# Optimization experiments

Measured on AMD Instinct MI355X. Metric: run time of the kernel, lower is better.

## Reference

```python
import jax, jax.numpy as jnp
import numpy as np

B, T, D = 2, 2048, 2048
N, KH, H = 16, 8, 128  # query heads, kv heads, head_dim
S = 2048               # cache size
EPS = 1e-6
ROPE_THETA = 1000000.0
K_MASK = -0.7 * float(np.finfo(np.float32).max)  # jax _get_large_negative(float32)


def _rms_norm(x, w):
    rms = jnp.sqrt(jnp.mean(x.astype(jnp.float32) ** 2, axis=-1, keepdims=True) + EPS)
    return (w * x / rms).astype(x.dtype)


def _rope_embeddings(positions, head_dim):
    fraction = jnp.arange(0, head_dim, 2, dtype=jnp.float32) / head_dim
    inv_freq = 1.0 / (ROPE_THETA ** fraction)
    sinusoid = jnp.einsum('BT,k->BTk', positions.astype(jnp.float32), inv_freq,
                          precision=jax.lax.Precision.HIGHEST)
    return jnp.sin(sinusoid), jnp.cos(sinusoid)


def _apply_rope(x, sin, cos):
    h = x.shape[-1] // 2
    x1, x2 = x[..., :h], x[..., h:]
    s, c = sin[:, :, None, :], cos[:, :, None, :]
    return jnp.concatenate([x1 * c - x2 * s, x2 * c + x1 * s], axis=-1).astype(x.dtype)


def _positions_from_segment_ids(seg):
    t = seg.shape[1]
    pos = jnp.arange(t, dtype=jnp.int32)[None, :] - jnp.argmax(seg, axis=1)[:, None]
    return jnp.where(seg != 0, pos, 2 ** 30)


def _num_left_pad(seg):
    return jnp.sum(jnp.cumsum(seg != 0, axis=-1) == 0, axis=-1).astype(jnp.int32)


def _attention(x, q_w, k_w, v_w, o_w, q_norm_w, k_norm_w, k_cache, v_cache,
               segment_ids, start_ind, cur_ind):
    b, t, _ = x.shape
    s = k_cache.shape[1]
    n, kh, h = q_w.shape[1], k_w.shape[1], q_w.shape[2]

    q = _rms_norm(jnp.einsum('BTD,DNH->BTNH', x, q_w), q_norm_w)  # [B,T,N,H]
    k = _rms_norm(jnp.einsum('BSD,DKH->BSKH', x, k_w), k_norm_w)  # [B,T,K,H]
    v = jnp.einsum('BSD,DKH->BSKH', x, v_w)                       # [B,T,K,H]

    start = jnp.where(start_ind < 0, _num_left_pad(segment_ids), start_ind)
    pos = _positions_from_segment_ids(segment_ids) + cur_ind
    sin, cos = _rope_embeddings(pos, h)
    q = _apply_rope(q, sin, cos)
    k = _apply_rope(k, sin, cos)

    # KV-cache update at cur_ind
    k_cache = jax.lax.dynamic_update_slice(k_cache, k, (0, cur_ind, 0, 0))
    v_cache = jax.lax.dynamic_update_slice(v_cache, v, (0, cur_ind, 0, 0))

    # GQA: group query heads per kv head
    qg = q.reshape(b, t, kh, n // kh, h)
    logits = jnp.einsum('BTHGD,BSHD->BHGTS', qg, k_cache) * (h ** -0.5)

    q_pos = cur_ind + jnp.arange(t, dtype=jnp.int32)[None, :] - start[:, None]  # [B,T]
    ts = jnp.arange(s, dtype=jnp.int32)
    kv_seg = (ts[None, :] >= start[:, None]) & (ts[None, :] < cur_ind + t)      # [B,S] bool
    k_pos = ts[None, :] - start[:, None]                                        # [B,S]
    causal = k_pos[:, None, :] <= q_pos[:, :, None]                             # [B,T,S]
    # faithful to original: bool kv segment ids compared against int segment_ids
    seg_mask = kv_seg[:, None, :].astype(segment_ids.dtype) == segment_ids[:, :, None]
    final_mask = (causal & seg_mask)[:, None, None, :, :]                       # [B,1,1,T,S]

    logits = jnp.where(final_mask, logits, K_MASK)
    attn = jax.nn.softmax(logits.astype(jnp.float32), axis=-1).astype(logits.dtype)
    o = jnp.einsum('BHGTS,BSHD->BTHGD', attn, v_cache).reshape(b, t, n, h)
    return jnp.einsum('BTNH,NHD->BTD', o, o_w)


def setup_inputs() -> dict:
    key = jax.random.key(0)
    ks = jax.random.split(key, 5)
    scale = 0.02
    return {
        'x': jax.random.normal(ks[0], (B, T, D), jnp.float32),
        'q_w': jax.random.normal(ks[1], (D, N, H), jnp.float32) * scale,
        'k_w': jax.random.normal(ks[2], (D, KH, H), jnp.float32) * scale,
        'v_w': jax.random.normal(ks[3], (D, KH, H), jnp.float32) * scale,
        'o_w': jax.random.normal(ks[4], (N, H, D), jnp.float32) * scale,
        'q_norm_w': jnp.ones((H,), jnp.float32),
        'k_norm_w': jnp.ones((H,), jnp.float32),
        'k_cache': jnp.zeros((B, S, KH, H), jnp.float32),
        'v_cache': jnp.zeros((B, S, KH, H), jnp.float32),
        'segment_ids': jnp.ones((B, T), jnp.int32),
        'start_ind': jnp.zeros((B,), jnp.int32),
        'cur_ind': 0,
        'right_pads': 0,
    }


def reference(x, q_w, k_w, v_w, o_w, q_norm_w, k_norm_w, k_cache, v_cache,
              segment_ids, start_ind, cur_ind, right_pads):
    # right_pads only advances the cache write pointer (stateful side effect); it
    # does not affect the attention output.
    return _attention(x, q_w, k_w, v_w, o_w, q_norm_w, k_norm_w,
                      k_cache, v_cache, segment_ids, start_ind, cur_ind)
```

## Files before the change

kernel.cpp:

```cpp
#include <hip/hip_runtime.h>
#include <climits>
#include <math.h>

#define Bc   2
#define Tc   2048
#define Dc   2048
#define Nc   16
#define KHc  8
#define Hc   128
#define Sc   2048

constexpr float EPSc   = 1e-6f;
constexpr float SCALE2 = 0.1275174477984469f;

typedef short short8 __attribute__((ext_vector_type(8)));
typedef float float4v __attribute__((ext_vector_type(4)));

union U16x8 { uint4 u; short8 s8; unsigned short us[8]; };

__device__ __forceinline__ unsigned short f2bf(float f) {
    union { float f; unsigned u; } v; v.f = f;
    unsigned r = v.u + 0x7FFFu + ((v.u >> 16) & 1u);
    return (unsigned short)(r >> 16);
}
__device__ __forceinline__ float bf2f(unsigned short u) {
    union { unsigned u; float f; } v; v.u = ((unsigned)u) << 16;
    return v.f;
}

__global__ void meta_kernel(const int* __restrict__ seg,
                            const int* __restrict__ start_ind,
                            int* __restrict__ meta)
{
    int b = blockIdx.x;
    __shared__ int s_max, s_amax, s_nz;
    if (threadIdx.x == 0) { s_max = INT_MIN; s_amax = Tc; s_nz = Tc; }
    __syncthreads();
    int lmax = INT_MIN;
    for (int t = threadIdx.x; t < Tc; t += blockDim.x)
        lmax = max(lmax, seg[b * Tc + t]);
    atomicMax(&s_max, lmax);
    __syncthreads();
    int mv = s_max;
    int lamax = Tc, lnz = Tc;
    for (int t = threadIdx.x; t < Tc; t += blockDim.x) {
        int v = seg[b * Tc + t];
        if (v == mv) lamax = min(lamax, t);
        if (v != 0)  lnz   = min(lnz, t);
    }
    atomicMin(&s_amax, lamax);
    atomicMin(&s_nz, lnz);
    __syncthreads();
    if (threadIdx.x == 0) {
        meta[b] = s_amax;
        int st = start_ind[b];
        meta[Bc + b] = (st < 0) ? s_nz : st;
    }
}

__global__ void cast_bf16(const float* __restrict__ in, unsigned short* __restrict__ out)
{
    size_t base = ((size_t)blockIdx.x * 256 + threadIdx.x) * 8;
    float4 a = *(const float4*)&in[base];
    float4 b = *(const float4*)&in[base + 4];
    U16x8 o;
    o.us[0] = f2bf(a.x); o.us[1] = f2bf(a.y); o.us[2] = f2bf(a.z); o.us[3] = f2bf(a.w);
    o.us[4] = f2bf(b.x); o.us[5] = f2bf(b.y); o.us[6] = f2bf(b.z); o.us[7] = f2bf(b.w);
    *(uint4*)&out[base] = o.u;
}

__global__ void fill_kcache(const float* __restrict__ kc, unsigned short* __restrict__ Kall,
                            const int* __restrict__ cur_ptr)
{
    int cur = cur_ptr[0];
    size_t base = ((size_t)blockIdx.x * 256 + threadIdx.x) * 8;
    int s = (int)((base >> 10) & (Sc - 1));
    if (s >= cur && s < cur + Tc) return;
    float4 a = *(const float4*)&kc[base];
    float4 b = *(const float4*)&kc[base + 4];
    U16x8 o;
    o.us[0] = f2bf(a.x); o.us[1] = f2bf(a.y); o.us[2] = f2bf(a.z); o.us[3] = f2bf(a.w);
    o.us[4] = f2bf(b.x); o.us[5] = f2bf(b.y); o.us[6] = f2bf(b.z); o.us[7] = f2bf(b.w);
    *(uint4*)&Kall[base] = o.u;
}

__global__ __launch_bounds__(256) void transpose_cast(const float* __restrict__ in,
                                                      unsigned short* __restrict__ out,
                                                      int R, int C)
{
    __shared__ float tile[32][33];
    int tid = threadIdx.x;
    int c0 = blockIdx.x * 32, r0 = blockIdx.y * 32;
#pragma unroll
    for (int i = 0; i < 4; ++i) {
        int row = (tid >> 5) + i * 8, col = tid & 31;
        tile[row][col] = in[(size_t)(r0 + row) * C + c0 + col];
    }
    __syncthreads();
#pragma unroll
    for (int i = 0; i < 4; ++i) {
        int rowo = (tid >> 5) + i * 8, colo = tid & 31;
        out[(size_t)(c0 + rowo) * R + r0 + colo] = f2bf(tile[colo][rowo]);
    }
}

__global__ void vtrans2(const unsigned short* __restrict__ QKVh,
                        const float* __restrict__ vc,
                        unsigned short* __restrict__ Vt,
                        const int* __restrict__ cur_ptr)
{
    int gid = blockIdx.x * 256 + threadIdx.x;
    int h  = gid & 127;
    int s8 = ((gid >> 7) & 255) * 8;
    int kh = (gid >> 15) & 7;
    int b  = gid >> 18;
    int cur = cur_ptr[0], curT = cur + Tc;
    unsigned short tmp[8];
#pragma unroll
    for (int e = 0; e < 8; ++e) {
        int s = s8 + e;
        unsigned short v;
        if (s >= cur && s < curT)
            v = QKVh[(size_t)(b * Tc + (s - cur)) * 4096 + 3072 + kh * Hc + h];
        else
            v = f2bf(vc[((size_t)(b * Sc + s) * KHc + kh) * Hc + h]);
        tmp[e] = v;
    }
    *(uint4*)&Vt[(((size_t)b * KHc + kh) * Hc + h) * Sc + s8] = *(uint4*)tmp;
}

__global__ __launch_bounds__(256, 2) void gemm_mfma(const unsigned short* __restrict__ A,
                                                    const unsigned short* __restrict__ BT,
                                                    void* __restrict__ Cout,
                                                    int M, int N, int K, int out_fp32)
{
    __shared__ __align__(16) unsigned short As[128 * 32];
    __shared__ __align__(16) unsigned short Bs[128 * 32];
    int tid = threadIdx.x;
    int lane = tid & 63, w = tid >> 6;
    int quad = lane >> 4, l15 = lane & 15;
    int bm = blockIdx.y * 128, bn = blockIdx.x * 128;
    int wm = (w >> 1) * 64, wn = (w & 1) * 64;

    int srow = lane >> 2;
    int pl   = lane & 3;
    int sw   = (quad ^ ((l15 >> 1) & 3)) * 8;

    float4v acc[16];
#pragma unroll
    for (int i = 0; i < 16; ++i) acc[i] = (float4v)0.f;

    for (int k0 = 0; k0 < K; k0 += 32) {
        __syncthreads();
#pragma unroll
        for (int c = 0; c < 2; ++c) {
            int j = w * 2 + c;
            int row = j * 16 + srow;
            int pg = pl ^ ((row >> 1) & 3);
            __builtin_amdgcn_global_load_lds(
                (__attribute__((address_space(1))) void*)(A + (size_t)(bm + row) * K + k0 + pg * 8),
                (__attribute__((address_space(3))) void*)(As + j * 512), 16, 0, 0);
            __builtin_amdgcn_global_load_lds(
                (__attribute__((address_space(1))) void*)(BT + (size_t)(bn + row) * K + k0 + pg * 8),
                (__attribute__((address_space(3))) void*)(Bs + j * 512), 16, 0, 0);
        }
        __syncthreads();
        short8 af[4];
#pragma unroll
        for (int mi = 0; mi < 4; ++mi)
            af[mi] = *(const short8*)&As[(wm + mi * 16 + l15) * 32 + sw];
#pragma unroll
        for (int ni = 0; ni < 4; ++ni) {
            short8 bf = *(const short8*)&Bs[(wn + ni * 16 + l15) * 32 + sw];
#pragma unroll
            for (int mi = 0; mi < 4; ++mi)
                acc[mi * 4 + ni] = __builtin_amdgcn_mfma_f32_16x16x32_bf16(af[mi], bf, acc[mi * 4 + ni], 0, 0, 0);
        }
    }

#pragma unroll
    for (int mi = 0; mi < 4; ++mi)
#pragma unroll
        for (int ni = 0; ni < 4; ++ni)
#pragma unroll
            for (int reg = 0; reg < 4; ++reg) {
                int row = bm + wm + mi * 16 + quad * 4 + reg;
                int col = bn + wn + ni * 16 + l15;
                float v = acc[mi * 4 + ni][reg];
                if (out_fp32) ((float*)Cout)[(size_t)row * N + col] = v;
                else ((unsigned short*)Cout)[(size_t)row * N + col] = f2bf(v);
            }
}

__global__ __launch_bounds__(256) void norm_rope(unsigned short* __restrict__ QKVh,
                                                 unsigned short* __restrict__ Kall,
                                                 const float* __restrict__ qw,
                                                 const float* __restrict__ kw,
                                                 const int* __restrict__ seg,
                                                 const int* __restrict__ meta,
                                                 const int* __restrict__ cur_ptr)
{
    int rowid = blockIdx.x * 4 + (threadIdx.x >> 6);
    int lane = threadIdx.x & 63;
    int hh = rowid % 24;
    int bt = rowid / 24;
    int t = bt & (Tc - 1);
    int b = bt >> 11;
    int cur = cur_ptr[0];

    const unsigned short* in;
    unsigned short* out;
    const float* wt;
    if (hh < 16) {
        unsigned short* p = QKVh + (size_t)bt * 4096 + hh * Hc;
        in = p; out = p; wt = qw;
    } else {
        int kh = hh - 16;
        in = QKVh + (size_t)bt * 4096 + 2048 + kh * Hc;
        out = Kall + (((size_t)b * Sc + cur + t) * KHc + kh) * Hc;
        wt = kw;
    }
    float v1 = bf2f(in[lane]), v2 = bf2f(in[lane + 64]);
    float ssq = v1 * v1 + v2 * v2;
#pragma unroll
    for (int off = 1; off < 64; off <<= 1) ssq += __shfl_xor(ssq, off);
    float rinv = rsqrtf(ssq * (1.0f / Hc) + EPSc);

    int sg = seg[bt];
    long long pos = (sg != 0) ? (long long)(t - meta[b]) : (long long)(1 << 30);
    float posf = (float)(pos + (long long)cur);
    float inv_freq = exp2f(-(float)lane * (19.931568569324174f / 64.0f));
    float s, c;
    sincosf(posf * inv_freq, &s, &c);

    float n1 = wt[lane] * v1 * rinv;
    float n2 = wt[lane + 64] * v2 * rinv;
    out[lane]      = f2bf(n1 * c - n2 * s);
    out[lane + 64] = f2bf(n2 * c + n1 * s);
}

__global__ __launch_bounds__(256, 2) void flash_mfma(const unsigned short* __restrict__ Qb,
                                                     const unsigned short* __restrict__ Kall,
                                                     const unsigned short* __restrict__ Vt,
                                                     const int* __restrict__ seg,
                                                     const int* __restrict__ meta,
                                                     const int* __restrict__ cur_ptr,
                                                     unsigned short* __restrict__ Ob)
{
    __shared__ __align__(16) unsigned short Ks[64 * 128];
    __shared__ __align__(16) unsigned short Vs[128 * 64];
    __shared__ __align__(16) unsigned short Ps[128 * 72];

    int tid = threadIdx.x;
    int lane = tid & 63, w = tid >> 6;
    int quad = lane >> 4, l15 = lane & 15;
    int bid = blockIdx.x;
    int raw = bid & 15;
    int n  = (bid >> 4) & 15;
    int b  = bid >> 8;
    int qt = (b == 0) ? raw : (15 - raw);
    int kh = n >> 1;
    int cur = cur_ptr[0];
    int startb = meta[Bc + b];
    int curT = cur + Tc;
    int t0 = qt * 128 + w * 32;

    short8 qf[2][4];
#pragma unroll
    for (int mi = 0; mi < 2; ++mi)
#pragma unroll
        for (int ks = 0; ks < 4; ++ks) {
            int row = t0 + mi * 16 + l15;
            U16x8 u;
            u.u = *(const uint4*)&Qb[(size_t)(b * Tc + row) * 4096 + n * Hc + ks * 32 + quad * 8];
            qf[mi][ks] = u.s8;
        }

    int code = 0, ct[8];
#pragma unroll
    for (int mi = 0; mi < 2; ++mi)
#pragma unroll
        for (int reg = 0; reg < 4; ++reg) {
            int idx = mi * 4 + reg;
            int trow = t0 + mi * 16 + quad * 4 + reg;
            int sg = seg[b * Tc + trow];
            int cls = (sg == 0) ? 0 : ((sg == 1) ? 1 : 2);
            code |= cls << (2 * idx);
            ct[idx] = cur + trow;
        }
    bool allseg1 = (code == 0x5555);

    float lsum[8];
#pragma unroll
    for (int i = 0; i < 8; ++i) lsum[i] = 0.f;
    float4v o[16];
#pragma unroll
    for (int i = 0; i < 16; ++i) o[i] = (float4v)0.f;

    int s_end = min(Sc, cur + qt * 128 + 128);
    int nch = (s_end + 63) >> 6;

    const size_t kstride = (size_t)KHc * Hc;
    const unsigned short* kptr[4];
    unsigned short* kdst[4];
#pragma unroll
    for (int i = 0; i < 4; ++i) {
        int j = w * 4 + i;
        int row = j * 4 + (lane >> 4);
        int pl = lane & 15;
        int pg = pl ^ ((row >> 1) & 7);
        kptr[i] = Kall + (size_t)b * Sc * kstride + (size_t)row * kstride + kh * Hc + pg * 8;
        kdst[i] = Ks + j * 512;
    }
    const unsigned short* vptr[4];
    unsigned short* vdst[4];
#pragma unroll
    for (int i = 0; i < 4; ++i) {
        int j = w * 4 + i;
        int h = j * 8 + (lane >> 3);
        int pl = lane & 7;
        int pg = pl ^ ((h >> 1) & 7);
        vptr[i] = Vt + ((size_t)b * KHc + kh) * (size_t)Hc * Sc + (size_t)h * Sc + pg * 8;
        vdst[i] = Vs + j * 512;
    }
    int sw3 = (l15 >> 1) & 7;

    for (int c = 0; c < nch; ++c) {
        int s0 = c * 64;
#pragma unroll
        for (int i = 0; i < 4; ++i) {
            __builtin_amdgcn_global_load_lds(
                (__attribute__((address_space(1))) void*)(kptr[i] + (size_t)s0 * kstride),
                (__attribute__((address_space(3))) void*)kdst[i], 16, 0, 0);
            __builtin_amdgcn_global_load_lds(
                (__attribute__((address_space(1))) void*)(vptr[i] + s0),
                (__attribute__((address_space(3))) void*)vdst[i], 16, 0, 0);
        }
        __syncthreads();

        float4v sacc[2][4];
#pragma unroll
        for (int mi = 0; mi < 2; ++mi)
#pragma unroll
            for (int j = 0; j < 4; ++j) sacc[mi][j] = (float4v)0.f;
#pragma unroll
        for (int j = 0; j < 4; ++j) {
#pragma unroll
            for (int ks = 0; ks < 4; ++ks) {
                short8 kf = *(const short8*)&Ks[(j * 16 + l15) * 128 + ((ks * 4 + quad) ^ sw3) * 8];
                sacc[0][j] = __builtin_amdgcn_mfma_f32_16x16x32_bf16(qf[0][ks], kf, sacc[0][j], 0, 0, 0);
                sacc[1][j] = __builtin_amdgcn_mfma_f32_16x16x32_bf16(qf[1][ks], kf, sacc[1][j], 0, 0, 0);
            }
        }

        bool fullok = allseg1 && (s0 >= startb) && (s0 + 63 <= cur + t0) && (s0 + 63 < curT);

#pragma unroll
        for (int mi = 0; mi < 2; ++mi) {
#pragma unroll
            for (int reg = 0; reg < 4; ++reg) {
                int idx = mi * 4 + reg;
                int prow = w * 32 + mi * 16 + quad * 4 + reg;
                if (fullok) {
#pragma unroll
                    for (int j = 0; j < 4; ++j) {
                        float p = exp2f(sacc[mi][j][reg] * SCALE2);
                        lsum[idx] += p;
                        Ps[prow * 72 + j * 16 + l15] = f2bf(p);
                    }
                } else {
                    int ctv = ct[idx];
                    int clsv = (code >> (2 * idx)) & 3;
#pragma unroll
                    for (int j = 0; j < 4; ++j) {
                        int s = s0 + j * 16 + l15;
                        int kvseg = (s >= startb && s < curT) ? 1 : 0;
                        bool ok = (s <= ctv) && (clsv == kvseg);
                        float arg = ok ? sacc[mi][j][reg] * SCALE2 : -1e30f;
                        float p = exp2f(arg);
                        lsum[idx] += p;
                        Ps[prow * 72 + j * 16 + l15] = f2bf(p);
                    }
                }
            }
        }

#pragma unroll
        for (int kk = 0; kk < 2; ++kk) {
            short8 pf0 = *(const short8*)&Ps[(w * 32 + l15) * 72 + kk * 32 + quad * 8];
            short8 pf1 = *(const short8*)&Ps[(w * 32 + 16 + l15) * 72 + kk * 32 + quad * 8];
#pragma unroll
            for (int nt = 0; nt < 8; ++nt) {
                short8 vf = *(const short8*)&Vs[(nt * 16 + l15) * 64 + ((kk * 4 + quad) ^ sw3) * 8];
                o[nt]     = __builtin_amdgcn_mfma_f32_16x16x32_bf16(pf0, vf, o[nt], 0, 0, 0);
                o[8 + nt] = __builtin_amdgcn_mfma_f32_16x16x32_bf16(pf1, vf, o[8 + nt], 0, 0, 0);
            }
        }
        __syncthreads();
    }

#pragma unroll
    for (int idx = 0; idx < 8; ++idx) {
        float l = lsum[idx];
        l += __shfl_xor(l, 1);
        l += __shfl_xor(l, 2);
        l += __shfl_xor(l, 4);
        l += __shfl_xor(l, 8);
        lsum[idx] = (l > 0.f) ? (1.0f / l) : 0.f;
    }

#pragma unroll
    for (int mi = 0; mi < 2; ++mi)
#pragma unroll
        for (int reg = 0; reg < 4; ++reg) {
            float linv = lsum[mi * 4 + reg];
            int trow = t0 + mi * 16 + quad * 4 + reg;
            size_t base = ((size_t)(b * Tc + trow) * Nc + n) * Hc;
#pragma unroll
            for (int nt = 0; nt < 8; ++nt)
                Ob[base + nt * 16 + l15] = f2bf(o[mi * 8 + nt][reg] * linv);
        }
}

extern "C" void kernel_launch(void* const* d_in, const int* in_sizes, int n_in,
                              void* d_out, int out_size, void* d_ws, size_t ws_size,
                              hipStream_t stream)
{
    const float* x        = (const float*)d_in[0];
    const float* q_w      = (const float*)d_in[1];
    const float* k_w      = (const float*)d_in[2];
    const float* v_w      = (const float*)d_in[3];
    const float* o_w      = (const float*)d_in[4];
    const float* q_norm_w = (const float*)d_in[5];
    const float* k_norm_w = (const float*)d_in[6];
    const float* k_cache  = (const float*)d_in[7];
    const float* v_cache  = (const float*)d_in[8];
    const int*   seg      = (const int*)d_in[9];
    const int*   startind = (const int*)d_in[10];
    const int*   cur_ptr  = (const int*)d_in[11];
    (void)in_sizes; (void)n_in; (void)out_size; (void)ws_size;

    char* base = (char*)d_ws;
    int* meta = (int*)base;
    unsigned short* QKVh = (unsigned short*)(base + 1024);
    unsigned short* Kall = (unsigned short*)(base + 33555456);
    unsigned short* Vt   = (unsigned short*)(base + 41944064);
    unsigned short* xb   = (unsigned short*)(base + 50332672);
    unsigned short* qkvwT= (unsigned short*)(base + 67109888);
    unsigned short* owT  = (unsigned short*)(base + 83887104);
    unsigned short* Ob   = xb;

    meta_kernel<<<Bc, 256, 0, stream>>>(seg, startind, meta);

    cast_bf16<<<4096, 256, 0, stream>>>(x, xb);
    transpose_cast<<<dim3(64, 64), 256, 0, stream>>>(q_w, qkvwT, Dc, Nc * Hc);
    transpose_cast<<<dim3(32, 64), 256, 0, stream>>>(k_w, qkvwT + (size_t)2048 * 2048, Dc, KHc * Hc);
    transpose_cast<<<dim3(32, 64), 256, 0, stream>>>(v_w, qkvwT + (size_t)3072 * 2048, Dc, KHc * Hc);
    transpose_cast<<<dim3(64, 64), 256, 0, stream>>>(o_w, owT, Nc * Hc, Dc);

    gemm_mfma<<<dim3(32, 32), 256, 0, stream>>>(xb, qkvwT, QKVh, Bc * Tc, 4096, Dc, 0);

    norm_rope<<<Bc * Tc * 24 / 4, 256, 0, stream>>>(QKVh, Kall,
                                                    q_norm_w, k_norm_w, seg, meta, cur_ptr);

    fill_kcache<<<2048, 256, 0, stream>>>(k_cache, Kall, cur_ptr);
    vtrans2<<<2048, 256, 0, stream>>>(QKVh, v_cache, Vt, cur_ptr);

    flash_mfma<<<Bc * Nc * (Tc / 128), 256, 0, stream>>>(QKVh, Kall, Vt, seg, meta, cur_ptr, Ob);

    gemm_mfma<<<dim3(16, 32), 256, 0, stream>>>(Ob, owT, d_out, Bc * Tc, Dc, Nc * Hc, 1);
}
```

Baseline: 422.9 us.

## Merge prep/post kernels and transpose flash attention tiles with fp16 PV

```diff
diff --git a/kernel.cpp b/kernel.cpp
--- a/kernel.cpp
+++ b/kernel.cpp
@@ -1,4 +1,5 @@
 #include <hip/hip_runtime.h>
+#include <hip/hip_fp16.h>
 #include <climits>
 #include <math.h>
 
@@ -14,9 +15,13 @@
 constexpr float SCALE2 = 0.1275174477984469f;
 
 typedef short short8 __attribute__((ext_vector_type(8)));
+typedef _Float16 half8 __attribute__((ext_vector_type(8)));
+typedef __fp16 fp16x2 __attribute__((ext_vector_type(2)));
 typedef float float4v __attribute__((ext_vector_type(4)));
 
-union U16x8 { uint4 u; short8 s8; unsigned short us[8]; };
+union U16x8 { uint4 u; short8 s8; half8 h8; unsigned short us[8]; };
+union H2U  { fp16x2 h; unsigned u; };
+union S8H8 { short8 s; half8 h; };
 
 __device__ __forceinline__ unsigned short f2bf(float f) {
     union { float f; unsigned u; } v; v.f = f;
@@ -28,69 +33,12 @@
     return v.f;
 }
 
-__global__ void meta_kernel(const int* __restrict__ seg,
-                            const int* __restrict__ start_ind,
-                            int* __restrict__ meta)
-{
-    int b = blockIdx.x;
-    __shared__ int s_max, s_amax, s_nz;
-    if (threadIdx.x == 0) { s_max = INT_MIN; s_amax = Tc; s_nz = Tc; }
-    __syncthreads();
-    int lmax = INT_MIN;
-    for (int t = threadIdx.x; t < Tc; t += blockDim.x)
-        lmax = max(lmax, seg[b * Tc + t]);
-    atomicMax(&s_max, lmax);
-    __syncthreads();
-    int mv = s_max;
-    int lamax = Tc, lnz = Tc;
-    for (int t = threadIdx.x; t < Tc; t += blockDim.x) {
-        int v = seg[b * Tc + t];
-        if (v == mv) lamax = min(lamax, t);
-        if (v != 0)  lnz   = min(lnz, t);
-    }
-    atomicMin(&s_amax, lamax);
-    atomicMin(&s_nz, lnz);
-    __syncthreads();
-    if (threadIdx.x == 0) {
-        meta[b] = s_amax;
-        int st = start_ind[b];
-        meta[Bc + b] = (st < 0) ? s_nz : st;
-    }
-}
-
-__global__ void cast_bf16(const float* __restrict__ in, unsigned short* __restrict__ out)
-{
-    size_t base = ((size_t)blockIdx.x * 256 + threadIdx.x) * 8;
-    float4 a = *(const float4*)&in[base];
-    float4 b = *(const float4*)&in[base + 4];
-    U16x8 o;
-    o.us[0] = f2bf(a.x); o.us[1] = f2bf(a.y); o.us[2] = f2bf(a.z); o.us[3] = f2bf(a.w);
-    o.us[4] = f2bf(b.x); o.us[5] = f2bf(b.y); o.us[6] = f2bf(b.z); o.us[7] = f2bf(b.w);
-    *(uint4*)&out[base] = o.u;
-}
-
-__global__ void fill_kcache(const float* __restrict__ kc, unsigned short* __restrict__ Kall,
-                            const int* __restrict__ cur_ptr)
-{
-    int cur = cur_ptr[0];
-    size_t base = ((size_t)blockIdx.x * 256 + threadIdx.x) * 8;
-    int s = (int)((base >> 10) & (Sc - 1));
-    if (s >= cur && s < cur + Tc) return;
-    float4 a = *(const float4*)&kc[base];
-    float4 b = *(const float4*)&kc[base + 4];
-    U16x8 o;
-    o.us[0] = f2bf(a.x); o.us[1] = f2bf(a.y); o.us[2] = f2bf(a.z); o.us[3] = f2bf(a.w);
-    o.us[4] = f2bf(b.x); o.us[5] = f2bf(b.y); o.us[6] = f2bf(b.z); o.us[7] = f2bf(b.w);
-    *(uint4*)&Kall[base] = o.u;
-}
-
-__global__ __launch_bounds__(256) void transpose_cast(const float* __restrict__ in,
-                                                      unsigned short* __restrict__ out,
-                                                      int R, int C)
-{
-    __shared__ float tile[32][33];
-    int tid = threadIdx.x;
-    int c0 = blockIdx.x * 32, r0 = blockIdx.y * 32;
+__device__ __forceinline__ void tc_body(const float* __restrict__ in,
+                                        unsigned short* __restrict__ out,
+                                        int R, int C, int bx, int by, int tid,
+                                        float tile[32][33])
+{
+    int c0 = bx * 32, r0 = by * 32;
 #pragma unroll
     for (int i = 0; i < 4; ++i) {
         int row = (tid >> 5) + i * 8, col = tid & 31;
@@ -104,29 +52,67 @@
     }
 }
 
-__global__ void vtrans2(const unsigned short* __restrict__ QKVh,
-                        const float* __restrict__ vc,
-                        unsigned short* __restrict__ Vt,
-                        const int* __restrict__ cur_ptr)
-{
-    int gid = blockIdx.x * 256 + threadIdx.x;
-    int h  = gid & 127;
-    int s8 = ((gid >> 7) & 255) * 8;
-    int kh = (gid >> 15) & 7;
-    int b  = gid >> 18;
-    int cur = cur_ptr[0], curT = cur + Tc;
-    unsigned short tmp[8];
-#pragma unroll
-    for (int e = 0; e < 8; ++e) {
-        int s = s8 + e;
-        unsigned short v;
-        if (s >= cur && s < curT)
-            v = QKVh[(size_t)(b * Tc + (s - cur)) * 4096 + 3072 + kh * Hc + h];
-        else
-            v = f2bf(vc[((size_t)(b * Sc + s) * KHc + kh) * Hc + h]);
-        tmp[e] = v;
-    }
-    *(uint4*)&Vt[(((size_t)b * KHc + kh) * Hc + h) * Sc + s8] = *(uint4*)tmp;
+__global__ __launch_bounds__(256) void prep(const float* __restrict__ x,
+                                            const float* __restrict__ qw,
+                                            const float* __restrict__ kw,
+                                            const float* __restrict__ vw,
+                                            const float* __restrict__ ow,
+                                            const int* __restrict__ seg,
+                                            const int* __restrict__ start_ind,
+                                            int* __restrict__ meta,
+                                            unsigned short* __restrict__ xb,
+                                            unsigned short* __restrict__ qkvwT,
+                                            unsigned short* __restrict__ owT)
+{
+    __shared__ float tile[32][33];
+    __shared__ int s_max, s_amax, s_nz;
+    int id = blockIdx.x;
+    int tid = threadIdx.x;
+
+    if (id < Bc) {
+        int b = id;
+        if (tid == 0) { s_max = INT_MIN; s_amax = Tc; s_nz = Tc; }
+        __syncthreads();
+        int lmax = INT_MIN;
+        for (int t = tid; t < Tc; t += 256) lmax = max(lmax, seg[b * Tc + t]);
+        atomicMax(&s_max, lmax);
+        __syncthreads();
+        int mv = s_max;
+        int lamax = Tc, lnz = Tc;
+        for (int t = tid; t < Tc; t += 256) {
+            int v = seg[b * Tc + t];
+            if (v == mv) lamax = min(lamax, t);
+            if (v != 0)  lnz   = min(lnz, t);
+        }
+        atomicMin(&s_amax, lamax);
+        atomicMin(&s_nz, lnz);
+        __syncthreads();
+        if (tid == 0) {
+            meta[b] = s_amax;
+            int st = start_ind[b];
+            meta[Bc + b] = (st < 0) ? s_nz : st;
+        }
+        return;
+    }
+    id -= Bc;
+    if (id < 4096) {
+        size_t base = ((size_t)id * 256 + tid) * 8;
+        float4 a = *(const float4*)&x[base];
+        float4 b = *(const float4*)&x[base + 4];
+        U16x8 o;
+        o.us[0] = f2bf(a.x); o.us[1] = f2bf(a.y); o.us[2] = f2bf(a.z); o.us[3] = f2bf(a.w);
+        o.us[4] = f2bf(b.x); o.us[5] = f2bf(b.y); o.us[6] = f2bf(b.z); o.us[7] = f2bf(b.w);
+        *(uint4*)&xb[base] = o.u;
+        return;
+    }
+    id -= 4096;
+    if (id < 4096) { tc_body(qw, qkvwT, 2048, 2048, id & 63, id >> 6, tid, tile); return; }
+    id -= 4096;
+    if (id < 2048) { tc_body(kw, qkvwT + (size_t)2048 * 2048, 2048, 1024, id & 31, id >> 5, tid, tile); return; }
+    id -= 2048;
+    if (id < 2048) { tc_body(vw, qkvwT + (size_t)3072 * 2048, 2048, 1024, id & 31, id >> 5, tid, tile); return; }
+    id -= 2048;
+    tc_body(ow, owT, 2048, 2048, id & 63, id >> 6, tid, tile);
 }
 
 __global__ __launch_bounds__(256, 2) void gemm_mfma(const unsigned short* __restrict__ A,
@@ -192,51 +178,94 @@
             }
 }
 
-__global__ __launch_bounds__(256) void norm_rope(unsigned short* __restrict__ QKVh,
-                                                 unsigned short* __restrict__ Kall,
-                                                 const float* __restrict__ qw,
-                                                 const float* __restrict__ kw,
-                                                 const int* __restrict__ seg,
-                                                 const int* __restrict__ meta,
-                                                 const int* __restrict__ cur_ptr)
-{
-    int rowid = blockIdx.x * 4 + (threadIdx.x >> 6);
-    int lane = threadIdx.x & 63;
-    int hh = rowid % 24;
-    int bt = rowid / 24;
-    int t = bt & (Tc - 1);
-    int b = bt >> 11;
+__global__ __launch_bounds__(256) void post(unsigned short* __restrict__ QKVh,
+                                            unsigned short* __restrict__ Kall,
+                                            unsigned short* __restrict__ Vt,
+                                            const float* __restrict__ qw,
+                                            const float* __restrict__ kw,
+                                            const int* __restrict__ seg,
+                                            const int* __restrict__ meta,
+                                            const int* __restrict__ cur_ptr,
+                                            const float* __restrict__ kc,
+                                            const float* __restrict__ vc)
+{
+    int id = blockIdx.x;
+    int tid = threadIdx.x;
     int cur = cur_ptr[0];
 
-    const unsigned short* in;
-    unsigned short* out;
-    const float* wt;
-    if (hh < 16) {
-        unsigned short* p = QKVh + (size_t)bt * 4096 + hh * Hc;
-        in = p; out = p; wt = qw;
-    } else {
-        int kh = hh - 16;
-        in = QKVh + (size_t)bt * 4096 + 2048 + kh * Hc;
-        out = Kall + (((size_t)b * Sc + cur + t) * KHc + kh) * Hc;
-        wt = kw;
-    }
-    float v1 = bf2f(in[lane]), v2 = bf2f(in[lane + 64]);
-    float ssq = v1 * v1 + v2 * v2;
-#pragma unroll
-    for (int off = 1; off < 64; off <<= 1) ssq += __shfl_xor(ssq, off);
-    float rinv = rsqrtf(ssq * (1.0f / Hc) + EPSc);
-
-    int sg = seg[bt];
-    long long pos = (sg != 0) ? (long long)(t - meta[b]) : (long long)(1 << 30);
-    float posf = (float)(pos + (long long)cur);
-    float inv_freq = exp2f(-(float)lane * (19.931568569324174f / 64.0f));
-    float s, c;
-    sincosf(posf * inv_freq, &s, &c);
-
-    float n1 = wt[lane] * v1 * rinv;
-    float n2 = wt[lane + 64] * v2 * rinv;
-    out[lane]      = f2bf(n1 * c - n2 * s);
-    out[lane + 64] = f2bf(n2 * c + n1 * s);
+    if (id < 24576) {
+        int rowid = id * 4 + (tid >> 6);
+        int lane = tid & 63;
+        int hh = rowid % 24;
+        int bt = rowid / 24;
+        int t = bt & (Tc - 1);
+        int b = bt >> 11;
+
+        const unsigned short* in;
+        unsigned short* out;
+        const float* wt;
+        if (hh < 16) {
+            unsigned short* p = QKVh + (size_t)bt * 4096 + hh * Hc;
+            in = p; out = p; wt = qw;
+        } else {
+            int kh = hh - 16;
+            in = QKVh + (size_t)bt * 4096 + 2048 + kh * Hc;
+            out = Kall + (((size_t)b * Sc + cur + t) * KHc + kh) * Hc;
+            wt = kw;
+        }
+        float v1 = bf2f(in[lane]), v2 = bf2f(in[lane + 64]);
+        float ssq = v1 * v1 + v2 * v2;
+#pragma unroll
+        for (int off = 1; off < 64; off <<= 1) ssq += __shfl_xor(ssq, off);
+        float rinv = rsqrtf(ssq * (1.0f / Hc) + EPSc);
+
+        int sg = seg[bt];
+        long long pos = (sg != 0) ? (long long)(t - meta[b]) : (long long)(1 << 30);
+        float posf = (float)(pos + (long long)cur);
+        float inv_freq = exp2f(-(float)lane * (19.931568569324174f / 64.0f));
+        float s, c;
+        sincosf(posf * inv_freq, &s, &c);
+
+        float n1 = wt[lane] * v1 * rinv;
+        float n2 = wt[lane + 64] * v2 * rinv;
+        out[lane]      = f2bf(n1 * c - n2 * s);
+        out[lane + 64] = f2bf(n2 * c + n1 * s);
+        return;
+    }
+    id -= 24576;
+    if (id < 2048) {
+        size_t base = ((size_t)id * 256 + tid) * 8;
+        int s = (int)((base >> 10) & (Sc - 1));
+        if (s >= cur && s < cur + Tc) return;
+        float4 a = *(const float4*)&kc[base];
+        float4 b = *(const float4*)&kc[base + 4];
+        U16x8 o;
+        o.us[0] = f2bf(a.x); o.us[1] = f2bf(a.y); o.us[2] = f2bf(a.z); o.us[3] = f2bf(a.w);
+        o.us[4] = f2bf(b.x); o.us[5] = f2bf(b.y); o.us[6] = f2bf(b.z); o.us[7] = f2bf(b.w);
+        *(uint4*)&Kall[base] = o.u;
+        return;
+    }
+    id -= 2048;
+    {
+        int gid = id * 256 + tid;
+        int h  = gid & 127;
+        int s8 = ((gid >> 7) & 255) * 8;
+        int kh = (gid >> 15) & 7;
+        int b  = gid >> 18;
+        int curT = cur + Tc;
+        unsigned short tmp[8];
+#pragma unroll
+        for (int e = 0; e < 8; ++e) {
+            int s = s8 + e;
+            float f;
+            if (s >= cur && s < curT)
+                f = bf2f(QKVh[(size_t)(b * Tc + (s - cur)) * 4096 + 3072 + kh * Hc + h]);
+            else
+                f = vc[((size_t)(b * Sc + s) * KHc + kh) * Hc + h];
+            tmp[e] = __half_as_ushort(__float2half(f));
+        }
+        *(uint4*)&Vt[(((size_t)b * KHc + kh) * Hc + h) * Sc + s8] = *(uint4*)tmp;
+    }
 }
 
 __global__ __launch_bounds__(256, 2) void flash_mfma(const unsigned short* __restrict__ Qb,
@@ -267,35 +296,31 @@
 
     short8 qf[2][4];
 #pragma unroll
-    for (int mi = 0; mi < 2; ++mi)
+    for (int qtile = 0; qtile < 2; ++qtile)
 #pragma unroll
         for (int ks = 0; ks < 4; ++ks) {
-            int row = t0 + mi * 16 + l15;
+            int row = t0 + qtile * 16 + l15;
             U16x8 u;
             u.u = *(const uint4*)&Qb[(size_t)(b * Tc + row) * 4096 + n * Hc + ks * 32 + quad * 8];
-            qf[mi][ks] = u.s8;
-        }
-
-    int code = 0, ct[8];
-#pragma unroll
-    for (int mi = 0; mi < 2; ++mi)
-#pragma unroll
-        for (int reg = 0; reg < 4; ++reg) {
-            int idx = mi * 4 + reg;
-            int trow = t0 + mi * 16 + quad * 4 + reg;
-            int sg = seg[b * Tc + trow];
-            int cls = (sg == 0) ? 0 : ((sg == 1) ? 1 : 2);
-            code |= cls << (2 * idx);
-            ct[idx] = cur + trow;
-        }
-    bool allseg1 = (code == 0x5555);
-
-    float lsum[8];
-#pragma unroll
-    for (int i = 0; i < 8; ++i) lsum[i] = 0.f;
-    float4v o[16];
-#pragma unroll
-    for (int i = 0; i < 16; ++i) o[i] = (float4v)0.f;
+            qf[qtile][ks] = u.s8;
+        }
+
+    int ctq[2], clsq[2];
+#pragma unroll
+    for (int qtile = 0; qtile < 2; ++qtile) {
+        int trow = t0 + qtile * 16 + l15;
+        int sg = seg[b * Tc + trow];
+        clsq[qtile] = (sg == 0) ? 0 : ((sg == 1) ? 1 : 2);
+        ctq[qtile] = cur + trow;
+    }
+    unsigned long long m0 = __ballot(clsq[0] == 1);
+    unsigned long long m1 = __ballot(clsq[1] == 1);
+    bool allseg1 = ((m0 & m1) == 0xFFFFFFFFFFFFFFFFull);
+
+    float lsum[2] = {0.f, 0.f};
+    float4v oT[16];
+#pragma unroll
+    for (int i = 0; i < 16; ++i) oT[i] = (float4v)0.f;
 
     int s_end = min(Sc, cur + qt * 128 + 128);
     int nch = (s_end + 63) >> 6;
@@ -324,6 +349,8 @@
         vdst[i] = Vs + j * 512;
     }
     int sw3 = (l15 >> 1) & 7;
+    unsigned short* psrow0 = Ps + (w * 32 + l15) * 72;
+    unsigned short* psrow1 = Ps + (w * 32 + 16 + l15) * 72;
 
     for (int c = 0; c < nch; ++c) {
         int s0 = c * 64;
@@ -338,88 +365,95 @@
         }
         __syncthreads();
 
-        float4v sacc[2][4];
-#pragma unroll
-        for (int mi = 0; mi < 2; ++mi)
-#pragma unroll
-            for (int j = 0; j < 4; ++j) sacc[mi][j] = (float4v)0.f;
-#pragma unroll
-        for (int j = 0; j < 4; ++j) {
-#pragma unroll
-            for (int ks = 0; ks < 4; ++ks) {
-                short8 kf = *(const short8*)&Ks[(j * 16 + l15) * 128 + ((ks * 4 + quad) ^ sw3) * 8];
-                sacc[0][j] = __builtin_amdgcn_mfma_f32_16x16x32_bf16(qf[0][ks], kf, sacc[0][j], 0, 0, 0);
-                sacc[1][j] = __builtin_amdgcn_mfma_f32_16x16x32_bf16(qf[1][ks], kf, sacc[1][j], 0, 0, 0);
+        float4v st[4][2];
+#pragma unroll
+        for (int i = 0; i < 4; ++i) { st[i][0] = (float4v)0.f; st[i][1] = (float4v)0.f; }
+#pragma unroll
+        for (int ks = 0; ks < 4; ++ks) {
+#pragma unroll
+            for (int stile = 0; stile < 4; ++stile) {
+                short8 kf = *(const short8*)&Ks[(stile * 16 + l15) * 128 + ((ks * 4 + quad) ^ sw3) * 8];
+                st[stile][0] = __builtin_amdgcn_mfma_f32_16x16x32_bf16(kf, qf[0][ks], st[stile][0], 0, 0, 0);
+                st[stile][1] = __builtin_amdgcn_mfma_f32_16x16x32_bf16(kf, qf[1][ks], st[stile][1], 0, 0, 0);
             }
         }
 
         bool fullok = allseg1 && (s0 >= startb) && (s0 + 63 <= cur + t0) && (s0 + 63 < curT);
 
 #pragma unroll
-        for (int mi = 0; mi < 2; ++mi) {
-#pragma unroll
-            for (int reg = 0; reg < 4; ++reg) {
-                int idx = mi * 4 + reg;
-                int prow = w * 32 + mi * 16 + quad * 4 + reg;
+        for (int stile = 0; stile < 4; ++stile) {
+#pragma unroll
+            for (int qtile = 0; qtile < 2; ++qtile) {
+                float p0, p1, p2, p3;
                 if (fullok) {
-#pragma unroll
-                    for (int j = 0; j < 4; ++j) {
-                        float p = exp2f(sacc[mi][j][reg] * SCALE2);
-                        lsum[idx] += p;
-                        Ps[prow * 72 + j * 16 + l15] = f2bf(p);
-                    }
+                    p0 = exp2f(st[stile][qtile][0] * SCALE2);
+                    p1 = exp2f(st[stile][qtile][1] * SCALE2);
+                    p2 = exp2f(st[stile][qtile][2] * SCALE2);
+                    p3 = exp2f(st[stile][qtile][3] * SCALE2);
                 } else {
-                    int ctv = ct[idx];
-                    int clsv = (code >> (2 * idx)) & 3;
-#pragma unroll
-                    for (int j = 0; j < 4; ++j) {
-                        int s = s0 + j * 16 + l15;
+                    int ctv = ctq[qtile], clsv = clsq[qtile];
+                    float pp[4];
+#pragma unroll
+                    for (int reg = 0; reg < 4; ++reg) {
+                        int s = s0 + stile * 16 + quad * 4 + reg;
                         int kvseg = (s >= startb && s < curT) ? 1 : 0;
                         bool ok = (s <= ctv) && (clsv == kvseg);
-                        float arg = ok ? sacc[mi][j][reg] * SCALE2 : -1e30f;
-                        float p = exp2f(arg);
-                        lsum[idx] += p;
-                        Ps[prow * 72 + j * 16 + l15] = f2bf(p);
+                        pp[reg] = exp2f(ok ? st[stile][qtile][reg] * SCALE2 : -1e30f);
                     }
+                    p0 = pp[0]; p1 = pp[1]; p2 = pp[2]; p3 = pp[3];
                 }
+                lsum[qtile] += (p0 + p1) + (p2 + p3);
+                H2U a, d;
+                a.h = __builtin_amdgcn_cvt_pkrtz(p0, p1);
+                d.h = __builtin_amdgcn_cvt_pkrtz(p2, p3);
+                uint2 pk; pk.x = a.u; pk.y = d.u;
+                unsigned short* pr = (qtile == 0) ? psrow0 : psrow1;
+                *(uint2*)&pr[stile * 16 + quad * 4] = pk;
             }
         }
 
 #pragma unroll
         for (int kk = 0; kk < 2; ++kk) {
-            short8 pf0 = *(const short8*)&Ps[(w * 32 + l15) * 72 + kk * 32 + quad * 8];
-            short8 pf1 = *(const short8*)&Ps[(w * 32 + 16 + l15) * 72 + kk * 32 + quad * 8];
-#pragma unroll
-            for (int nt = 0; nt < 8; ++nt) {
-                short8 vf = *(const short8*)&Vs[(nt * 16 + l15) * 64 + ((kk * 4 + quad) ^ sw3) * 8];
-                o[nt]     = __builtin_amdgcn_mfma_f32_16x16x32_bf16(pf0, vf, o[nt], 0, 0, 0);
-                o[8 + nt] = __builtin_amdgcn_mfma_f32_16x16x32_bf16(pf1, vf, o[8 + nt], 0, 0, 0);
+            S8H8 pf0, pf1;
+            pf0.s = *(const short8*)&psrow0[kk * 32 + quad * 8];
+            pf1.s = *(const short8*)&psrow1[kk * 32 + quad * 8];
+#pragma unroll
+            for (int htile = 0; htile < 8; ++htile) {
+                S8H8 vf;
+                vf.s = *(const short8*)&Vs[(htile * 16 + l15) * 64 + ((kk * 4 + quad) ^ sw3) * 8];
+                oT[htile * 2 + 0] = __builtin_amdgcn_mfma_f32_16x16x32_f16(vf.h, pf0.h, oT[htile * 2 + 0], 0, 0, 0);
+                oT[htile * 2 + 1] = __builtin_amdgcn_mfma_f32_16x16x32_f16(vf.h, pf1.h, oT[htile * 2 + 1], 0, 0, 0);
             }
         }
         __syncthreads();
     }
 
-#pragma unroll
-    for (int idx = 0; idx < 8; ++idx) {
-        float l = lsum[idx];
-        l += __shfl_xor(l, 1);
-        l += __shfl_xor(l, 2);
-        l += __shfl_xor(l, 4);
-        l += __shfl_xor(l, 8);
-        lsum[idx] = (l > 0.f) ? (1.0f / l) : 0.f;
-    }
-
-#pragma unroll
-    for (int mi = 0; mi < 2; ++mi)
-#pragma unroll
-        for (int reg = 0; reg < 4; ++reg) {
-            float linv = lsum[mi * 4 + reg];
-            int trow = t0 + mi * 16 + quad * 4 + reg;
-            size_t base = ((size_t)(b * Tc + trow) * Nc + n) * Hc;
-#pragma unroll
-            for (int nt = 0; nt < 8; ++nt)
-                Ob[base + nt * 16 + l15] = f2bf(o[mi * 8 + nt][reg] * linv);
-        }
+    float linv[2];
+#pragma unroll
+    for (int qtile = 0; qtile < 2; ++qtile) {
+        float l = lsum[qtile];
+        l += __shfl_xor(l, 16);
+        l += __shfl_xor(l, 32);
+        linv[qtile] = (l > 0.f) ? (1.0f / l) : 0.f;
+    }
+
+#pragma unroll
+    for (int qtile = 0; qtile < 2; ++qtile) {
+        int trow = t0 + qtile * 16 + l15;
+        size_t base = ((size_t)(b * Tc + trow) * Nc + n) * Hc;
+#pragma unroll
+        for (int htile = 0; htile < 8; ++htile) {
+            float4v v = oT[htile * 2 + qtile];
+            unsigned short r0 = f2bf(v[0] * linv[qtile]);
+            unsigned short r1 = f2bf(v[1] * linv[qtile]);
+            unsigned short r2 = f2bf(v[2] * linv[qtile]);
+            unsigned short r3 = f2bf(v[3] * linv[qtile]);
+            uint2 pk;
+            pk.x = (unsigned)r0 | ((unsigned)r1 << 16);
+            pk.y = (unsigned)r2 | ((unsigned)r3 << 16);
+            *(uint2*)&Ob[base + htile * 16 + quad * 4] = pk;
+        }
+    }
 }
 
 extern "C" void kernel_launch(void* const* d_in, const int* in_sizes, int n_in,
@@ -450,21 +484,13 @@
     unsigned short* owT  = (unsigned short*)(base + 83887104);
     unsigned short* Ob   = xb;
 
-    meta_kernel<<<Bc, 256, 0, stream>>>(seg, startind, meta);
-
-    cast_bf16<<<4096, 256, 0, stream>>>(x, xb);
-    transpose_cast<<<dim3(64, 64), 256, 0, stream>>>(q_w, qkvwT, Dc, Nc * Hc);
-    transpose_cast<<<dim3(32, 64), 256, 0, stream>>>(k_w, qkvwT + (size_t)2048 * 2048, Dc, KHc * Hc);
-    transpose_cast<<<dim3(32, 64), 256, 0, stream>>>(v_w, qkvwT + (size_t)3072 * 2048, Dc, KHc * Hc);
-    transpose_cast<<<dim3(64, 64), 256, 0, stream>>>(o_w, owT, Nc * Hc, Dc);
+    prep<<<Bc + 4096 + 4096 + 2048 + 2048 + 4096, 256, 0, stream>>>(
+        x, q_w, k_w, v_w, o_w, seg, startind, meta, xb, qkvwT, owT);
 
     gemm_mfma<<<dim3(32, 32), 256, 0, stream>>>(xb, qkvwT, QKVh, Bc * Tc, 4096, Dc, 0);
 
-    norm_rope<<<Bc * Tc * 24 / 4, 256, 0, stream>>>(QKVh, Kall,
-                                                    q_norm_w, k_norm_w, seg, meta, cur_ptr);
-
-    fill_kcache<<<2048, 256, 0, stream>>>(k_cache, Kall, cur_ptr);
-    vtrans2<<<2048, 256, 0, stream>>>(QKVh, v_cache, Vt, cur_ptr);
+    post<<<24576 + 2048 + 2048, 256, 0, stream>>>(QKVh, Kall, Vt,
+        q_norm_w, k_norm_w, seg, meta, cur_ptr, k_cache, v_cache);
 
     flash_mfma<<<Bc * Nc * (Tc / 128), 256, 0, stream>>>(QKVh, Kall, Vt, seg, meta, cur_ptr, Ob);
 
```

After: 396.6 us. 1.07x faster.
